# Performance work log

Measured on AMD Instinct MI355X. Metric: run time of the kernel, lower is better.

Reference implementation:

```python
import jax, jax.numpy as jnp
import numpy as np

B, T, F, H, E = 32, 512, 64, 64, 32  # batch, time, features(=sequence_length), hidden_dim, encoding_size


def setup_inputs() -> dict:
    key = jax.random.key(0)
    ks = jax.random.split(key, 14)
    sc = 0.05
    return {
        "x": jax.random.normal(ks[0], (B, T, F), jnp.float32),
        "s": jax.random.normal(ks[1], (B, T, E), jnp.float32),
        # gating FFN params
        "ffn_w1": jax.random.normal(ks[2], (F, H), jnp.float32) * sc,
        "ffn_b1": jnp.zeros((H,), jnp.float32),
        "ffn_w2": jax.random.normal(ks[3], (E, H), jnp.float32) * sc,
        "ffn_b2": jnp.zeros((H,), jnp.float32),
        "ffn_w3": jax.random.normal(ks[4], (H, F), jnp.float32) * sc,
        "ffn_b3": jnp.zeros((F,), jnp.float32),
        # per-feature expert FFN_j params (F experts, each Dense(1->H), ELU, Dense(H->H))
        "exp_w1": jax.random.normal(ks[5], (F, H), jnp.float32) * sc,  # weight of Dense(1->H) per feature
        "exp_b1": jnp.zeros((F, H), jnp.float32),
        "exp_w3": jax.random.normal(ks[6], (F, H, H), jnp.float32) * sc,
        "exp_b3": jnp.zeros((F, H), jnp.float32),
    }


def reference(x, s, ffn_w1, ffn_b1, ffn_w2, ffn_b2, ffn_w3, ffn_b3,
              exp_w1, exp_b1, exp_w3, exp_b3):
    # gating network: softmax over feature axis
    g = jnp.einsum('btf,fh->bth', x, ffn_w1) + ffn_b1 \
        + jnp.einsum('bte,eh->bth', s, ffn_w2) + ffn_b2
    logits = jnp.einsum('bth,hf->btf', jax.nn.elu(g), ffn_w3) + ffn_b3
    w_t = jax.nn.softmax(logits, axis=2)  # [B,T,F]

    # per-feature experts, batched: Dense(1->H) is a rank-1 outer product
    h = jax.nn.elu(x[..., None] * exp_w1[None, None] + exp_b1[None, None])  # [B,T,F,H]
    expert_out = jnp.einsum('btfh,fhk->btfk', h, exp_w3) + exp_b3[None, None]  # [B,T,F,H]

    # gate-weighted sum over features
    return jnp.einsum('btfk,btf->btk', expert_out, w_t)  # [B,T,H]
```

## Files before the change

### kernel.cpp

```cpp
#include <hip/hip_runtime.h>
#include <hip/hip_bf16.h>
#include <math.h>

#define NTOK 16384
#define LOG2E 1.44269504088896340736f
#define LN2   0.69314718055994530942f

typedef __attribute__((ext_vector_type(8))) short short8;
typedef __attribute__((ext_vector_type(4))) float f32x4;

__device__ __forceinline__ unsigned pack_bf16(float a, float b) {
    union { __hip_bfloat162 h; unsigned u; } cv;
    cv.h = __float22bfloat162_rn(make_float2(a, b));
    return cv.u;
}
__device__ __forceinline__ unsigned pk_bf16(float a, float b) {
    unsigned r;
    asm("v_cvt_pk_bf16_f32 %0, %1, %2" : "=v"(r) : "v"(a), "v"(b));
    return r;
}
__device__ __forceinline__ float exp2_hw(float x) {
#if __has_builtin(__builtin_amdgcn_exp2f)
    return __builtin_amdgcn_exp2f(x);
#else
    return __expf(x * LN2);
#endif
}
__device__ __forceinline__ float eluf(float z) {
    return z > 0.0f ? z : (__expf(z) - 1.0f);
}

__device__ __forceinline__ void agen16t(const float* __restrict__ wb,
                                        float xv, float wt, float wtln2,
                                        short8& A0, short8& A1) {
    auto site = [&](float w, float b) -> float {
        const float z2 = fmaf(xv, w, b);
        const float e  = exp2_hw(fminf(z2, 0.0f));
        return fmaf(wtln2, fmaxf(z2, 0.0f), fmaf(wt, e, -wt));
    };
    {
        const float4 wa  = *(const float4*)(wb);
        const float4 wv2 = *(const float4*)(wb + 4);
        const float4 ba  = *(const float4*)(wb + 64);
        const float4 bb  = *(const float4*)(wb + 68);
        uint4 v0;
        v0.x = pk_bf16(site(wa.x,  ba.x), site(wa.y,  ba.y));
        v0.y = pk_bf16(site(wa.z,  ba.z), site(wa.w,  ba.w));
        v0.z = pk_bf16(site(wv2.x, bb.x), site(wv2.y, bb.y));
        v0.w = pk_bf16(site(wv2.z, bb.z), site(wv2.w, bb.w));
        A0 = *(short8*)&v0;
    }
    {
        const float4 wc = *(const float4*)(wb + 32);
        const float4 wd = *(const float4*)(wb + 36);
        const float4 bc = *(const float4*)(wb + 96);
        const float4 bd = *(const float4*)(wb + 100);
        uint4 v1;
        v1.x = pk_bf16(site(wc.x, bc.x), site(wc.y, bc.y));
        v1.y = pk_bf16(site(wc.z, bc.z), site(wc.w, bc.w));
        v1.z = pk_bf16(site(wd.x, bd.x), site(wd.y, bd.y));
        v1.w = pk_bf16(site(wd.z, bd.z), site(wd.w, bd.w));
        A1 = *(short8*)&v1;
    }
}

__global__ __launch_bounds__(256)
void prepass(const float* __restrict__ ew3, const float* __restrict__ eb3,
             unsigned short* __restrict__ ws) {
    __shared__ float tile[64 * 65];
    const int bid = blockIdx.x, tid = threadIdx.x;
    const float* src = (bid < 64) ? (ew3 + (size_t)bid * 4096) : eb3;

    const int r = tid >> 2, c0 = (tid & 3) * 16;
    #pragma unroll
    for (int j = 0; j < 4; ++j) {
        float4 v = *(const float4*)(src + r * 64 + c0 + j * 4);
        tile[r * 65 + c0 + j * 4 + 0] = v.x;
        tile[r * 65 + c0 + j * 4 + 1] = v.y;
        tile[r * 65 + c0 + j * 4 + 2] = v.z;
        tile[r * 65 + c0 + j * 4 + 3] = v.w;
    }
    __syncthreads();

    uint4* dst = (uint4*)(ws + (size_t)bid * 4096);
    #pragma unroll
    for (int it = 0; it < 2; ++it) {
        const int idx = tid + it * 256;
        const int c = idx >> 8, u = (idx >> 6) & 3, l = idx & 63;
        const int mm = l & 15, q = (l >> 4) & 3;
        const int rb = c * 32 + q * 8, col = u * 16 + mm;
        unsigned pw[4];
        #pragma unroll
        for (int p = 0; p < 4; ++p)
            pw[p] = pack_bf16(tile[(rb + 2 * p) * 65 + col],
                              tile[(rb + 2 * p + 1) * 65 + col]);
        uint4 pk; pk.x = pw[0]; pk.y = pw[1]; pk.z = pw[2]; pk.w = pw[3];
        dst[idx] = pk;
    }
}

__global__ __launch_bounds__(256)
void prep_gate(const float* __restrict__ ew3, const float* __restrict__ eb3,
               const float* __restrict__ x,   const float* __restrict__ s,
               const float* __restrict__ fw1, const float* __restrict__ fb1,
               const float* __restrict__ fw2, const float* __restrict__ fb2,
               const float* __restrict__ fw3, const float* __restrict__ fb3,
               unsigned short* __restrict__ img, float* __restrict__ wtg)
{
    __shared__ float smem[64 * 65];
    const int tid = threadIdx.x;

    if (blockIdx.x < 65) {
        const int bid = blockIdx.x;
        const float* src = (bid < 64) ? (ew3 + (size_t)bid * 4096) : eb3;
        const int r = tid >> 2, c0 = (tid & 3) * 16;
        #pragma unroll
        for (int j = 0; j < 4; ++j) {
            float4 v = *(const float4*)(src + r * 64 + c0 + j * 4);
            smem[r * 65 + c0 + j * 4 + 0] = v.x;
            smem[r * 65 + c0 + j * 4 + 1] = v.y;
            smem[r * 65 + c0 + j * 4 + 2] = v.z;
            smem[r * 65 + c0 + j * 4 + 3] = v.w;
        }
        __syncthreads();
        uint4* dst = (uint4*)(img + (size_t)bid * 4096);
        #pragma unroll
        for (int it = 0; it < 2; ++it) {
            const int idx = tid + it * 256;
            const int c = idx >> 8, u = (idx >> 6) & 3, l = idx & 63;
            const int mm = l & 15, q = (l >> 4) & 3;
            const int rb = c * 32 + q * 8, col = u * 16 + mm;
            unsigned pw[4];
            #pragma unroll
            for (int p = 0; p < 4; ++p)
                pw[p] = pack_bf16(smem[(rb + 2 * p) * 65 + col],
                                  smem[(rb + 2 * p + 1) * 65 + col]);
            uint4 pk; pk.x = pw[0]; pk.y = pw[1]; pk.z = pw[2]; pk.w = pw[3];
            dst[idx] = pk;
        }
        return;
    }

    float* xls = smem;
    float* egs = smem + 16 * 68;
    const int gb = blockIdx.x - 65;
    const int tokbase = gb * 16;
    const int wv = tid >> 6, lane = tid & 63;

    {
        const int t = tid >> 4, fq = (tid & 15) * 4;
        *(float4*)&xls[t * 68 + fq] =
            *(const float4*)(x + (size_t)(tokbase + t) * 64 + fq);
    }
    __syncthreads();

    const int t0w = wv * 4;
    const float* sw = s + (size_t)(tokbase + t0w) * 32;
    float g[4];
    const float b0 = fb1[lane] + fb2[lane];
    #pragma unroll
    for (int t = 0; t < 4; ++t) g[t] = b0;
    #pragma unroll 2
    for (int f = 0; f < 64; f += 4) {
        const float w0 = fw1[(f + 0) * 64 + lane];
        const float w1 = fw1[(f + 1) * 64 + lane];
        const float w2 = fw1[(f + 2) * 64 + lane];
        const float w3v = fw1[(f + 3) * 64 + lane];
        #pragma unroll
        for (int t = 0; t < 4; ++t) {
            const float4 xa = *(const float4*)&xls[(t0w + t) * 68 + f];
            g[t] = fmaf(xa.x, w0, fmaf(xa.y, w1, fmaf(xa.z, w2, fmaf(xa.w, w3v, g[t]))));
        }
    }
    #pragma unroll 2
    for (int e = 0; e < 32; e += 4) {
        const float w0 = fw2[(e + 0) * 64 + lane];
        const float w1 = fw2[(e + 1) * 64 + lane];
        const float w2 = fw2[(e + 2) * 64 + lane];
        const float w3v = fw2[(e + 3) * 64 + lane];
        #pragma unroll
        for (int t = 0; t < 4; ++t) {
            const float4 sa = *(const float4*)(sw + t * 32 + e);
            g[t] = fmaf(sa.x, w0, fmaf(sa.y, w1, fmaf(sa.z, w2, fmaf(sa.w, w3v, g[t]))));
        }
    }
    #pragma unroll
    for (int t = 0; t < 4; ++t) egs[(t0w + t) * 64 + lane] = eluf(g[t]);

    float lg[4];
    const float b3 = fb3[lane];
    #pragma unroll
    for (int t = 0; t < 4; ++t) lg[t] = b3;
    #pragma unroll 2
    for (int h = 0; h < 64; h += 4) {
        const float w0 = fw3[(h + 0) * 64 + lane];
        const float w1 = fw3[(h + 1) * 64 + lane];
        const float w2 = fw3[(h + 2) * 64 + lane];
        const float w3v = fw3[(h + 3) * 64 + lane];
        #pragma unroll
        for (int t = 0; t < 4; ++t) {
            const float4 ev = *(const float4*)&egs[(t0w + t) * 64 + h];
            lg[t] = fmaf(ev.x, w0, fmaf(ev.y, w1, fmaf(ev.z, w2, fmaf(ev.w, w3v, lg[t]))));
        }
    }
    #pragma unroll
    for (int t = 0; t < 4; ++t) {
        float mx = lg[t];
        #pragma unroll
        for (int off = 32; off > 0; off >>= 1) mx = fmaxf(mx, __shfl_xor(mx, off));
        const float p = __expf(lg[t] - mx);
        float sm = p;
        #pragma unroll
        for (int off = 32; off > 0; off >>= 1) sm += __shfl_xor(sm, off);
        wtg[(size_t)(tokbase + t0w + t) * 64 + lane] = p / sm;
    }
}

__global__ __launch_bounds__(512, 4)
void moe_main8(const float* __restrict__ x,
               const float* __restrict__ ew1, const float* __restrict__ eb1,
               const unsigned short* __restrict__ img,
               const float* __restrict__ wtg,
               float* __restrict__ out)
{
    __shared__ __align__(16) float xls[32 * 68];
    __shared__ __align__(16) float wls[32 * 68];
    __shared__ __align__(16) float wbped[64 * 128];

    const int tid = threadIdx.x;
    const int wv = tid >> 6, lane = tid & 63;
    const int m = tid & 15, quad = (tid >> 4) & 3;
    const int tile = wv & 1, g = wv >> 1;
    const int f0 = g * 16;
    const int trow = tile * 16 + m;
    const int tokbase = blockIdx.x * 32;

    {
        const int t = tid >> 4, fq = (tid & 15) * 4;
        *(float4*)&xls[t * 68 + fq] =
            *(const float4*)(x + (size_t)(tokbase + t) * 64 + fq);
        *(float4*)&wls[t * 68 + fq] =
            *(const float4*)(wtg + (size_t)(tokbase + t) * 64 + fq);
        #pragma unroll
        for (int k = 0; k < 2; ++k) {
            const int idx = tid + k * 512;
            const int fr = idx >> 4, c4 = (idx & 15) * 4;
            float4 wv4 = *(const float4*)(ew1 + fr * 64 + c4);
            float4 bv4 = *(const float4*)(eb1 + fr * 64 + c4);
            wv4.x *= LOG2E; wv4.y *= LOG2E; wv4.z *= LOG2E; wv4.w *= LOG2E;
            bv4.x *= LOG2E; bv4.y *= LOG2E; bv4.z *= LOG2E; bv4.w *= LOG2E;
            *(float4*)&wbped[fr * 128 + c4]      = wv4;
            *(float4*)&wbped[fr * 128 + 64 + c4] = bv4;
        }
    }
    __syncthreads();

    f32x4 acc[4];
    #pragma unroll
    for (int u = 0; u < 4; ++u) acc[u] = (f32x4){0.f, 0.f, 0.f, 0.f};

    const uint4* bp = (const uint4*)img + (size_t)f0 * 512 + lane;
    uint4 B0[8], B1[8];
    #pragma unroll
    for (int j = 0; j < 8; ++j) B0[j] = bp[j * 64];
    bp += 512;

    const float* xp    = &xls[trow * 68 + f0];
    const float* wp    = &wls[trow * 68 + f0];
    const float* wbase = &wbped[f0 * 128 + quad * 8];
    float xvA = xp[0], wtA = wp[0], wlA = wtA * LN2;

    #pragma unroll 1
    for (int p = 0; p < 8; ++p) {
        #pragma unroll
        for (int j = 0; j < 8; ++j) B1[j] = bp[j * 64];
        bp += 512;
        const float xvB = xp[1], wtB = wp[1], wlB = wtB * LN2;
        {
            short8 a0, a1;
            agen16t(wbase, xvA, wtA, wlA, a0, a1);
            acc[0] = __builtin_amdgcn_mfma_f32_16x16x32_bf16(a0, *(short8*)&B0[0], acc[0], 0, 0, 0);
            acc[1] = __builtin_amdgcn_mfma_f32_16x16x32_bf16(a0, *(short8*)&B0[1], acc[1], 0, 0, 0);
            acc[2] = __builtin_amdgcn_mfma_f32_16x16x32_bf16(a0, *(short8*)&B0[2], acc[2], 0, 0, 0);
            acc[3] = __builtin_amdgcn_mfma_f32_16x16x32_bf16(a0, *(short8*)&B0[3], acc[3], 0, 0, 0);
            acc[0] = __builtin_amdgcn_mfma_f32_16x16x32_bf16(a1, *(short8*)&B0[4], acc[0], 0, 0, 0);
            acc[1] = __builtin_amdgcn_mfma_f32_16x16x32_bf16(a1, *(short8*)&B0[5], acc[1], 0, 0, 0);
            acc[2] = __builtin_amdgcn_mfma_f32_16x16x32_bf16(a1, *(short8*)&B0[6], acc[2], 0, 0, 0);
            acc[3] = __builtin_amdgcn_mfma_f32_16x16x32_bf16(a1, *(short8*)&B0[7], acc[3], 0, 0, 0);
        }
        wbase += 128;

        #pragma unroll
        for (int j = 0; j < 8; ++j) B0[j] = bp[j * 64];
        bp += 512;
        xvA = xp[2]; wtA = wp[2]; wlA = wtA * LN2;
        {
            short8 a0, a1;
            agen16t(wbase, xvB, wtB, wlB, a0, a1);
            acc[0] = __builtin_amdgcn_mfma_f32_16x16x32_bf16(a0, *(short8*)&B1[0], acc[0], 0, 0, 0);
            acc[1] = __builtin_amdgcn_mfma_f32_16x16x32_bf16(a0, *(short8*)&B1[1], acc[1], 0, 0, 0);
            acc[2] = __builtin_amdgcn_mfma_f32_16x16x32_bf16(a0, *(short8*)&B1[2], acc[2], 0, 0, 0);
            acc[3] = __builtin_amdgcn_mfma_f32_16x16x32_bf16(a0, *(short8*)&B1[3], acc[3], 0, 0, 0);
            acc[0] = __builtin_amdgcn_mfma_f32_16x16x32_bf16(a1, *(short8*)&B1[4], acc[0], 0, 0, 0);
            acc[1] = __builtin_amdgcn_mfma_f32_16x16x32_bf16(a1, *(short8*)&B1[5], acc[1], 0, 0, 0);
            acc[2] = __builtin_amdgcn_mfma_f32_16x16x32_bf16(a1, *(short8*)&B1[6], acc[2], 0, 0, 0);
            acc[3] = __builtin_amdgcn_mfma_f32_16x16x32_bf16(a1, *(short8*)&B1[7], acc[3], 0, 0, 0);
        }
        wbase += 128; xp += 2; wp += 2;
    }

    if (wv < 4) {
        const int eh = g;
        const int e0 = eh * 32 + quad * 8;
        uint4 av;
        av.x = pk_bf16(wls[trow * 68 + e0 + 0], wls[trow * 68 + e0 + 1]);
        av.y = pk_bf16(wls[trow * 68 + e0 + 2], wls[trow * 68 + e0 + 3]);
        av.z = pk_bf16(wls[trow * 68 + e0 + 4], wls[trow * 68 + e0 + 5]);
        av.w = pk_bf16(wls[trow * 68 + e0 + 6], wls[trow * 68 + e0 + 7]);
        const short8 a = *(short8*)&av;
        const uint4* bq = (const uint4*)img + (size_t)64 * 512 + lane;
        #pragma unroll
        for (int u = 0; u < 4; ++u) {
            uint4 bv = bq[eh * 256 + u * 64];
            acc[u] = __builtin_amdgcn_mfma_f32_16x16x32_bf16(a, *(short8*)&bv, acc[u], 0, 0, 0);
        }
    }

    __syncthreads();
    if (g >= 2) {
        float* p = wbped + tile * 2176 + (g - 2) * 1088;
        #pragma unroll
        for (int u = 0; u < 4; ++u)
            #pragma unroll
            for (int r = 0; r < 4; ++r)
                p[(quad * 4 + r) * 68 + u * 16 + m] = acc[u][r];
    }
    __syncthreads();
    if (g < 2) {
        const float* p = wbped + tile * 2176 + g * 1088;
        #pragma unroll
        for (int u = 0; u < 4; ++u)
            #pragma unroll
            for (int r = 0; r < 4; ++r)
                acc[u][r] += p[(quad * 4 + r) * 68 + u * 16 + m];
    }
    __syncthreads();
    if (g == 1) {
        float* p = wbped + tile * 2176;
        #pragma unroll
        for (int u = 0; u < 4; ++u)
            #pragma unroll
            for (int r = 0; r < 4; ++r)
                p[(quad * 4 + r) * 68 + u * 16 + m] = acc[u][r];
    }
    __syncthreads();
    if (g == 0) {
        float* p = wbped + tile * 2176;
        #pragma unroll
        for (int u = 0; u < 4; ++u)
            #pragma unroll
            for (int r = 0; r < 4; ++r) {
                const int idx = (quad * 4 + r) * 68 + u * 16 + m;
                p[idx] += acc[u][r];
            }
    }
    __syncthreads();

    {
        const int t = tid >> 4, kq = tid & 15;
        const float* srcp = wbped + (t >> 4) * 2176 + (t & 15) * 68 + kq * 4;
        *(float4*)(out + (size_t)(tokbase + t) * 64 + kq * 4) = *(const float4*)srcp;
    }
}

__global__ __launch_bounds__(512, 4)
void moe_main(const float* __restrict__ x,   const float* __restrict__ s,
              const float* __restrict__ fw1, const float* __restrict__ fb1,
              const float* __restrict__ fw2, const float* __restrict__ fb2,
              const float* __restrict__ fw3, const float* __restrict__ fb3,
              const float* __restrict__ ew1, const float* __restrict__ eb1,
              const float* __restrict__ ew3, const float* __restrict__ eb3,
              const unsigned short* __restrict__ img,
              float* __restrict__ out)
{
    __shared__ __align__(16) float xls[32 * 68];
    __shared__ __align__(16) float wts[32 * 65];
    __shared__ __align__(16) float egs[32 * 64];
    __shared__ __align__(16) float ped0[4][16 * 68];
    __shared__ __align__(16) float ped1[4][16 * 68];

    const int tid = threadIdx.x;
    const int wv = tid >> 6, lane = tid & 63;
    const int m = tid & 15, quad = (tid >> 4) & 3;
    const int tokbase = blockIdx.x * 32;

    {
        const int t = tid >> 4, fq = (tid & 15) * 4;
        *(float4*)&xls[t * 68 + fq] =
            *(const float4*)(x + (size_t)(tokbase + t) * 64 + fq);
    }
    __syncthreads();

    {
        const int t0w = wv * 4;
        const float* sw = s + (size_t)(tokbase + t0w) * 32;
        float g[4];
        const float b0 = fb1[lane] + fb2[lane];
        #pragma unroll
        for (int t = 0; t < 4; ++t) g[t] = b0;
        for (int f = 0; f < 64; f += 4) {
            const float w0 = fw1[(f + 0) * 64 + lane];
            const float w1 = fw1[(f + 1) * 64 + lane];
            const float w2 = fw1[(f + 2) * 64 + lane];
            const float w3v = fw1[(f + 3) * 64 + lane];
            #pragma unroll
            for (int t = 0; t < 4; ++t) {
                const float4 xa = *(const float4*)&xls[(t0w + t) * 68 + f];
                g[t] = fmaf(xa.x, w0, fmaf(xa.y, w1, fmaf(xa.z, w2, fmaf(xa.w, w3v, g[t]))));
            }
        }
        for (int e = 0; e < 32; e += 4) {
            const float w0 = fw2[(e + 0) * 64 + lane];
            const float w1 = fw2[(e + 1) * 64 + lane];
            const float w2 = fw2[(e + 2) * 64 + lane];
            const float w3v = fw2[(e + 3) * 64 + lane];
            #pragma unroll
            for (int t = 0; t < 4; ++t) {
                const float4 sa = *(const float4*)(sw + t * 32 + e);
                g[t] = fmaf(sa.x, w0, fmaf(sa.y, w1, fmaf(sa.z, w2, fmaf(sa.w, w3v, g[t]))));
            }
        }
        #pragma unroll
        for (int t = 0; t < 4; ++t) egs[(t0w + t) * 64 + lane] = eluf(g[t]);

        float lg[4];
        const float b3 = fb3[lane];
        #pragma unroll
        for (int t = 0; t < 4; ++t) lg[t] = b3;
        for (int h = 0; h < 64; h += 4) {
            const float w0 = fw3[(h + 0) * 64 + lane];
            const float w1 = fw3[(h + 1) * 64 + lane];
            const float w2 = fw3[(h + 2) * 64 + lane];
            const float w3v = fw3[(h + 3) * 64 + lane];
            #pragma unroll
            for (int t = 0; t < 4; ++t) {
                const float4 ev = *(const float4*)&egs[(t0w + t) * 64 + h];
                lg[t] = fmaf(ev.x, w0, fmaf(ev.y, w1, fmaf(ev.z, w2, fmaf(ev.w, w3v, lg[t]))));
            }
        }
        #pragma unroll
        for (int t = 0; t < 4; ++t) {
            float mx = lg[t];
            #pragma unroll
            for (int off = 32; off > 0; off >>= 1) mx = fmaxf(mx, __shfl_xor(mx, off));
            const float p = __expf(lg[t] - mx);
            float sm = p;
            #pragma unroll
            for (int off = 32; off > 0; off >>= 1) sm += __shfl_xor(sm, off);
            wts[(t0w + t) * 65 + lane] = p / sm;
        }
    }
    __syncthreads();

    const int f0 = wv * 8;
    f32x4 acc0[4], acc1[4];
    #pragma unroll
    for (int u = 0; u < 4; ++u) {
        acc0[u] = (f32x4){0.f, 0.f, 0.f, 0.f};
        acc1[u] = (f32x4){0.f, 0.f, 0.f, 0.f};
    }

    const uint4* bp = (const uint4*)img + (size_t)f0 * 512 + lane;
    uint4  B[2][8];
    float4 W[2][4];
    float4 Bb[2][4];
    float  XV[2][2];
    float  WT[2][2];

    #pragma unroll
    for (int i = 0; i < 8; ++i) B[0][i] = bp[(i >> 2) * 256 + (i & 3) * 64];
    bp += 512;
    #pragma unroll
    for (int c = 0; c < 2; ++c) {
        W[0][c * 2 + 0]  = *(const float4*)(ew1 + f0 * 64 + c * 32 + quad * 8);
        W[0][c * 2 + 1]  = *(const float4*)(ew1 + f0 * 64 + c * 32 + quad * 8 + 4);
        Bb[0][c * 2 + 0] = *(const float4*)(eb1 + f0 * 64 + c * 32 + quad * 8);
        Bb[0][c * 2 + 1] = *(const float4*)(eb1 + f0 * 64 + c * 32 + quad * 8 + 4);
    }
    XV[0][0] = xls[m * 68 + f0];        WT[0][0] = wts[m * 65 + f0];
    XV[0][1] = xls[(16 + m) * 68 + f0]; WT[0][1] = wts[(16 + m) * 65 + f0];

    #pragma unroll
    for (int ff = 0; ff < 8; ++ff) {
        const int cur = ff & 1, nxt = cur ^ 1;
        if (ff < 7) {
            const int fn = f0 + ff + 1;
            #pragma unroll
            for (int i = 0; i < 8; ++i) B[nxt][i] = bp[(i >> 2) * 256 + (i & 3) * 64];
            bp += 512;
            #pragma unroll
            for (int c = 0; c < 2; ++c) {
                W[nxt][c * 2 + 0]  = *(const float4*)(ew1 + fn * 64 + c * 32 + quad * 8);
                W[nxt][c * 2 + 1]  = *(const float4*)(ew1 + fn * 64 + c * 32 + quad * 8 + 4);
                Bb[nxt][c * 2 + 0] = *(const float4*)(eb1 + fn * 64 + c * 32 + quad * 8);
                Bb[nxt][c * 2 + 1] = *(const float4*)(eb1 + fn * 64 + c * 32 + quad * 8 + 4);
            }
            XV[nxt][0] = xls[m * 68 + fn];        WT[nxt][0] = wts[m * 65 + fn];
            XV[nxt][1] = xls[(16 + m) * 68 + fn]; WT[nxt][1] = wts[(16 + m) * 65 + fn];
        }
        const float xv0 = XV[cur][0], wt0 = WT[cur][0];
        const float xv1 = XV[cur][1], wt1 = WT[cur][1];
        short8 a0[2], a1[2];
        #pragma unroll
        for (int c = 0; c < 2; ++c) {
            const float4 wa = W[cur][c * 2 + 0],  wb = W[cur][c * 2 + 1];
            const float4 ba = Bb[cur][c * 2 + 0], bb = Bb[cur][c * 2 + 1];
            uint4 v0, v1;
            v0.x = pack_bf16(wt0 * eluf(fmaf(xv0, wa.x, ba.x)),
                             wt0 * eluf(fmaf(xv0, wa.y, ba.y)));
            v0.y = pack_bf16(wt0 * eluf(fmaf(xv0, wa.z, ba.z)),
                             wt0 * eluf(fmaf(xv0, wa.w, ba.w)));
            v0.z = pack_bf16(wt0 * eluf(fmaf(xv0, wb.x, bb.x)),
                             wt0 * eluf(fmaf(xv0, wb.y, bb.y)));
            v0.w = pack_bf16(wt0 * eluf(fmaf(xv0, wb.z, bb.z)),
                             wt0 * eluf(fmaf(xv0, wb.w, bb.w)));
            v1.x = pack_bf16(wt1 * eluf(fmaf(xv1, wa.x, ba.x)),
                             wt1 * eluf(fmaf(xv1, wa.y, ba.y)));
            v1.y = pack_bf16(wt1 * eluf(fmaf(xv1, wa.z, ba.z)),
                             wt1 * eluf(fmaf(xv1, wa.w, ba.w)));
            v1.z = pack_bf16(wt1 * eluf(fmaf(xv1, wb.x, bb.x)),
                             wt1 * eluf(fmaf(xv1, wb.y, bb.y)));
            v1.w = pack_bf16(wt1 * eluf(fmaf(xv1, wb.z, bb.z)),
                             wt1 * eluf(fmaf(xv1, wb.w, bb.w)));
            a0[c] = *(short8*)&v0;
            a1[c] = *(short8*)&v1;
        }
        acc0[0] = __builtin_amdgcn_mfma_f32_16x16x32_bf16(a0[0], *(short8*)&B[cur][0], acc0[0], 0, 0, 0);
        acc0[1] = __builtin_amdgcn_mfma_f32_16x16x32_bf16(a0[0], *(short8*)&B[cur][1], acc0[1], 0, 0, 0);
        acc0[2] = __builtin_amdgcn_mfma_f32_16x16x32_bf16(a0[0], *(short8*)&B[cur][2], acc0[2], 0, 0, 0);
        acc0[3] = __builtin_amdgcn_mfma_f32_16x16x32_bf16(a0[0], *(short8*)&B[cur][3], acc0[3], 0, 0, 0);
        acc1[0] = __builtin_amdgcn_mfma_f32_16x16x32_bf16(a1[0], *(short8*)&B[cur][0], acc1[0], 0, 0, 0);
        acc1[1] = __builtin_amdgcn_mfma_f32_16x16x32_bf16(a1[0], *(short8*)&B[cur][1], acc1[1], 0, 0, 0);
        acc1[2] = __builtin_amdgcn_mfma_f32_16x16x32_bf16(a1[0], *(short8*)&B[cur][2], acc1[2], 0, 0, 0);
        acc1[3] = __builtin_amdgcn_mfma_f32_16x16x32_bf16(a1[0], *(short8*)&B[cur][3], acc1[3], 0, 0, 0);
        acc0[0] = __builtin_amdgcn_mfma_f32_16x16x32_bf16(a0[1], *(short8*)&B[cur][4], acc0[0], 0, 0, 0);
        acc0[1] = __builtin_amdgcn_mfma_f32_16x16x32_bf16(a0[1], *(short8*)&B[cur][5], acc0[1], 0, 0, 0);
        acc0[2] = __builtin_amdgcn_mfma_f32_16x16x32_bf16(a0[1], *(short8*)&B[cur][6], acc0[2], 0, 0, 0);
        acc0[3] = __builtin_amdgcn_mfma_f32_16x16x32_bf16(a0[1], *(short8*)&B[cur][7], acc0[3], 0, 0, 0);
        acc1[0] = __builtin_amdgcn_mfma_f32_16x16x32_bf16(a1[1], *(short8*)&B[cur][4], acc1[0], 0, 0, 0);
        acc1[1] = __builtin_amdgcn_mfma_f32_16x16x32_bf16(a1[1], *(short8*)&B[cur][5], acc1[1], 0, 0, 0);
        acc1[2] = __builtin_amdgcn_mfma_f32_16x16x32_bf16(a1[1], *(short8*)&B[cur][6], acc1[2], 0, 0, 0);
        acc1[3] = __builtin_amdgcn_mfma_f32_16x16x32_bf16(a1[1], *(short8*)&B[cur][7], acc1[3], 0, 0, 0);
    }

    if (wv < 4) {
        const int tile = wv >> 1, eh = wv & 1;
        const int e0 = eh * 32 + quad * 8;
        const int trow = tile * 16 + m;
        uint4 av;
        av.x = pack_bf16(wts[trow * 65 + e0 + 0], wts[trow * 65 + e0 + 1]);
        av.y = pack_bf16(wts[trow * 65 + e0 + 2], wts[trow * 65 + e0 + 3]);
        av.z = pack_bf16(wts[trow * 65 + e0 + 4], wts[trow * 65 + e0 + 5]);
        av.w = pack_bf16(wts[trow * 65 + e0 + 6], wts[trow * 65 + e0 + 7]);
        short8 a = *(short8*)&av;
        const uint4* bq = (const uint4*)img + (size_t)64 * 512;
        if (tile == 0) {
            #pragma unroll
            for (int u = 0; u < 4; ++u) {
                uint4 bv = bq[eh * 256 + u * 64 + lane];
                acc0[u] = __builtin_amdgcn_mfma_f32_16x16x32_bf16(a, *(short8*)&bv, acc0[u], 0, 0, 0);
            }
        } else {
            #pragma unroll
            for (int u = 0; u < 4; ++u) {
                uint4 bv = bq[eh * 256 + u * 64 + lane];
                acc1[u] = __builtin_amdgcn_mfma_f32_16x16x32_bf16(a, *(short8*)&bv, acc1[u], 0, 0, 0);
            }
        }
    }

    if (wv >= 4) {
        #pragma unroll
        for (int u = 0; u < 4; ++u)
            #pragma unroll
            for (int r = 0; r < 4; ++r) {
                const int idx = (quad * 4 + r) * 68 + u * 16 + m;
                ped0[wv - 4][idx] = acc0[u][r];
                ped1[wv - 4][idx] = acc1[u][r];
            }
    }
    __syncthreads();
    if (wv < 4) {
        #pragma unroll
        for (int u = 0; u < 4; ++u)
            #pragma unroll
            for (int r = 0; r < 4; ++r) {
                const int idx = (quad * 4 + r) * 68 + u * 16 + m;
                acc0[u][r] += ped0[wv][idx];
                acc1[u][r] += ped1[wv][idx];
            }
    }
    __syncthreads();
    if (wv == 2 || wv == 3) {
        #pragma unroll
        for (int u = 0; u < 4; ++u)
            #pragma unroll
            for (int r = 0; r < 4; ++r) {
                const int idx = (quad * 4 + r) * 68 + u * 16 + m;
                ped0[wv - 2][idx] = acc0[u][r];
                ped1[wv - 2][idx] = acc1[u][r];
            }
    }
    __syncthreads();
    if (wv < 2) {
        #pragma unroll
        for (int u = 0; u < 4; ++u)
            #pragma unroll
            for (int r = 0; r < 4; ++r) {
                const int idx = (quad * 4 + r) * 68 + u * 16 + m;
                acc0[u][r] += ped0[wv][idx];
                acc1[u][r] += ped1[wv][idx];
            }
    }
    __syncthreads();
    if (wv == 1) {
        #pragma unroll
        for (int u = 0; u < 4; ++u)
            #pragma unroll
            for (int r = 0; r < 4; ++r) {
                const int idx = (quad * 4 + r) * 68 + u * 16 + m;
                ped0[0][idx] = acc0[u][r];
                ped1[0][idx] = acc1[u][r];
            }
    }
    __syncthreads();
    if (wv == 0) {
        #pragma unroll
        for (int u = 0; u < 4; ++u)
            #pragma unroll
            for (int r = 0; r < 4; ++r) {
                const int idx = (quad * 4 + r) * 68 + u * 16 + m;
                ped0[0][idx] += acc0[u][r];
                ped1[0][idx] += acc1[u][r];
            }
    }
    __syncthreads();

    {
        const int t = tid >> 4, kq = tid & 15;
        const float* srcp = (t < 16) ? &ped0[0][t * 68 + kq * 4]
                                     : &ped1[0][(t - 16) * 68 + kq * 4];
        *(float4*)(out + (size_t)(tokbase + t) * 64 + kq * 4) = *(const float4*)srcp;
    }
}

__device__ __forceinline__ void gen_a_fb(const float* __restrict__ ew1,
                                         const float* __restrict__ eb1,
                                         int f, int quad, float xv, float wt,
                                         short8* a) {
    #pragma unroll
    for (int c = 0; c < 2; ++c) {
        const float* w1p = ew1 + f * 64 + c * 32 + quad * 8;
        const float* b1p = eb1 + f * 64 + c * 32 + quad * 8;
        const float4 w1a = *(const float4*)w1p, w1b = *(const float4*)(w1p + 4);
        const float4 b1a = *(const float4*)b1p, b1b = *(const float4*)(b1p + 4);
        uint4 av;
        av.x = pack_bf16(wt * eluf(fmaf(xv, w1a.x, b1a.x)),
                         wt * eluf(fmaf(xv, w1a.y, b1a.y)));
        av.y = pack_bf16(wt * eluf(fmaf(xv, w1a.z, b1a.z)),
                         wt * eluf(fmaf(xv, w1a.w, b1a.w)));
        av.z = pack_bf16(wt * eluf(fmaf(xv, w1b.x, b1b.x)),
                         wt * eluf(fmaf(xv, w1b.y, b1b.y)));
        av.w = pack_bf16(wt * eluf(fmaf(xv, w1b.z, b1b.z)),
                         wt * eluf(fmaf(xv, w1b.w, b1b.w)));
        a[c] = *(short8*)&av;
    }
}
__device__ __forceinline__ void gen_b_fp32(const float* __restrict__ w3f,
                                           int quad, int m, short8 b[2][4]) {
    #pragma unroll
    for (int c = 0; c < 2; ++c)
        #pragma unroll
        for (int u = 0; u < 4; ++u) {
            const float* wp = w3f + (size_t)(c * 32 + quad * 8) * 64 + u * 16 + m;
            uint4 v;
            v.x = pack_bf16(wp[0],   wp[64]);
            v.y = pack_bf16(wp[128], wp[192]);
            v.z = pack_bf16(wp[256], wp[320]);
            v.w = pack_bf16(wp[384], wp[448]);
            b[c][u] = *(short8*)&v;
        }
}

__global__ __launch_bounds__(512, 8)
void moe_fb(const float* __restrict__ x,   const float* __restrict__ s,
            const float* __restrict__ fw1, const float* __restrict__ fb1,
            const float* __restrict__ fw2, const float* __restrict__ fb2,
            const float* __restrict__ fw3, const float* __restrict__ fb3,
            const float* __restrict__ ew1, const float* __restrict__ eb1,
            const float* __restrict__ ew3, const float* __restrict__ eb3,
            float* __restrict__ out)
{
    __shared__ __align__(16) float xls[16 * 68];
    __shared__ __align__(16) float wts[16 * 65];
    __shared__ __align__(16) float egs[16 * 64];
    __shared__ __align__(16) float ped[4][16 * 68];

    const int tid = threadIdx.x;
    const int wv = tid >> 6, lane = tid & 63;
    const int tokbase = blockIdx.x * 16;

    if (tid < 256) {
        const int t = tid >> 4, fq = (tid & 15) * 4;
        *(float4*)&xls[t * 68 + fq] =
            *(const float4*)(x + (size_t)(tokbase + t) * 64 + fq);
    }
    __syncthreads();
    {
        const int t0w = wv * 2;
        const float* sw = s + (size_t)(tokbase + t0w) * 32;
        float g0, g1;
        g0 = g1 = fb1[lane] + fb2[lane];
        for (int ff = 0; ff < 64; ff += 4) {
            const float4 xa = *(const float4*)&xls[(t0w + 0) * 68 + ff];
            const float4 xb = *(const float4*)&xls[(t0w + 1) * 68 + ff];
            const float w0 = fw1[(ff + 0) * 64 + lane];
            const float w1 = fw1[(ff + 1) * 64 + lane];
            const float w2 = fw1[(ff + 2) * 64 + lane];
            const float w3v = fw1[(ff + 3) * 64 + lane];
            g0 = fmaf(xa.x, w0, fmaf(xa.y, w1, fmaf(xa.z, w2, fmaf(xa.w, w3v, g0))));
            g1 = fmaf(xb.x, w0, fmaf(xb.y, w1, fmaf(xb.z, w2, fmaf(xb.w, w3v, g1))));
        }
        for (int e = 0; e < 32; e += 4) {
            const float4 sa = *(const float4*)(sw + e);
            const float4 sb = *(const float4*)(sw + 32 + e);
            const float w0 = fw2[(e + 0) * 64 + lane];
            const float w1 = fw2[(e + 1) * 64 + lane];
            const float w2 = fw2[(e + 2) * 64 + lane];
            const float w3v = fw2[(e + 3) * 64 + lane];
            g0 = fmaf(sa.x, w0, fmaf(sa.y, w1, fmaf(sa.z, w2, fmaf(sa.w, w3v, g0))));
            g1 = fmaf(sb.x, w0, fmaf(sb.y, w1, fmaf(sb.z, w2, fmaf(sb.w, w3v, g1))));
        }
        egs[(t0w + 0) * 64 + lane] = eluf(g0);
        egs[(t0w + 1) * 64 + lane] = eluf(g1);
        float lg0 = fb3[lane], lg1 = lg0;
        for (int h = 0; h < 64; h += 4) {
            const float4 e0 = *(const float4*)&egs[(t0w + 0) * 64 + h];
            const float4 e1 = *(const float4*)&egs[(t0w + 1) * 64 + h];
            const float w0 = fw3[(h + 0) * 64 + lane];
            const float w1 = fw3[(h + 1) * 64 + lane];
            const float w2 = fw3[(h + 2) * 64 + lane];
            const float w3v = fw3[(h + 3) * 64 + lane];
            lg0 = fmaf(e0.x, w0, fmaf(e0.y, w1, fmaf(e0.z, w2, fmaf(e0.w, w3v, lg0))));
            lg1 = fmaf(e1.x, w0, fmaf(e1.y, w1, fmaf(e1.z, w2, fmaf(e1.w, w3v, lg1))));
        }
        float mx0 = lg0, mx1 = lg1;
        #pragma unroll
        for (int off = 32; off > 0; off >>= 1) {
            mx0 = fmaxf(mx0, __shfl_xor(mx0, off));
            mx1 = fmaxf(mx1, __shfl_xor(mx1, off));
        }
        const float p0 = __expf(lg0 - mx0), p1 = __expf(lg1 - mx1);
        float s0 = p0, s1 = p1;
        #pragma unroll
        for (int off = 32; off > 0; off >>= 1) {
            s0 += __shfl_xor(s0, off);
            s1 += __shfl_xor(s1, off);
        }
        wts[(t0w + 0) * 65 + lane] = p0 / s0;
        wts[(t0w + 1) * 65 + lane] = p1 / s1;
    }
    __syncthreads();

    const int m = tid & 15, quad = (tid >> 4) & 3;
    const int f0 = wv * 8;
    f32x4 acc[4];
    #pragma unroll
    for (int u = 0; u < 4; ++u) acc[u] = (f32x4){0.f, 0.f, 0.f, 0.f};

    #pragma unroll
    for (int ff = 0; ff < 8; ++ff) {
        const int fcur = f0 + ff;
        short8 b[2][4], a[2];
        gen_b_fp32(ew3 + (size_t)fcur * 4096, quad, m, b);
        gen_a_fb(ew1, eb1, fcur, quad, xls[m * 68 + fcur], wts[m * 65 + fcur], a);
        #pragma unroll
        for (int u = 0; u < 4; ++u) {
            acc[u] = __builtin_amdgcn_mfma_f32_16x16x32_bf16(a[0], b[0][u], acc[u], 0, 0, 0);
            acc[u] = __builtin_amdgcn_mfma_f32_16x16x32_bf16(a[1], b[1][u], acc[u], 0, 0, 0);
        }
    }
    if (wv < 2) {
        const int e0 = wv * 32 + quad * 8;
        uint4 av;
        av.x = pack_bf16(wts[m * 65 + e0 + 0], wts[m * 65 + e0 + 1]);
        av.y = pack_bf16(wts[m * 65 + e0 + 2], wts[m * 65 + e0 + 3]);
        av.z = pack_bf16(wts[m * 65 + e0 + 4], wts[m * 65 + e0 + 5]);
        av.w = pack_bf16(wts[m * 65 + e0 + 6], wts[m * 65 + e0 + 7]);
        short8 a = *(short8*)&av;
        #pragma unroll
        for (int u = 0; u < 4; ++u) {
            const float* wp = eb3 + (size_t)e0 * 64 + u * 16 + m;
            uint4 bv;
            bv.x = pack_bf16(wp[0],   wp[64]);
            bv.y = pack_bf16(wp[128], wp[192]);
            bv.z = pack_bf16(wp[256], wp[320]);
            bv.w = pack_bf16(wp[384], wp[448]);
            acc[u] = __builtin_amdgcn_mfma_f32_16x16x32_bf16(a, *(short8*)&bv, acc[u], 0, 0, 0);
        }
    }
    if (wv >= 4) {
        #pragma unroll
        for (int u = 0; u < 4; ++u)
            #pragma unroll
            for (int r = 0; r < 4; ++r)
                ped[wv - 4][(quad * 4 + r) * 68 + u * 16 + m] = acc[u][r];
    }
    __syncthreads();
    if (wv < 4) {
        #pragma unroll
        for (int u = 0; u < 4; ++u)
            #pragma unroll
            for (int r = 0; r < 4; ++r)
                acc[u][r] += ped[wv][(quad * 4 + r) * 68 + u * 16 + m];
    }
    __syncthreads();
    if (wv == 2 || wv == 3) {
        #pragma unroll
        for (int u = 0; u < 4; ++u)
            #pragma unroll
            for (int r = 0; r < 4; ++r)
                ped[wv - 2][(quad * 4 + r) * 68 + u * 16 + m] = acc[u][r];
    }
    __syncthreads();
    if (wv < 2) {
        #pragma unroll
        for (int u = 0; u < 4; ++u)
            #pragma unroll
            for (int r = 0; r < 4; ++r)
                acc[u][r] += ped[wv][(quad * 4 + r) * 68 + u * 16 + m];
    }
    __syncthreads();
    if (wv == 1) {
        #pragma unroll
        for (int u = 0; u < 4; ++u)
            #pragma unroll
            for (int r = 0; r < 4; ++r)
                ped[0][(quad * 4 + r) * 68 + u * 16 + m] = acc[u][r];
    }
    __syncthreads();
    if (wv == 0) {
        #pragma unroll
        for (int u = 0; u < 4; ++u)
            #pragma unroll
            for (int r = 0; r < 4; ++r)
                ped[0][(quad * 4 + r) * 68 + u * 16 + m] += acc[u][r];
    }
    __syncthreads();
    if (tid < 256) {
        const int t = tid >> 4, kq = tid & 15;
        float4 o = *(const float4*)&ped[0][t * 68 + kq * 4];
        *(float4*)(out + (size_t)(tokbase + t) * 64 + kq * 4) = o;
    }
}

extern "C" void kernel_launch(void* const* d_in, const int* in_sizes, int n_in,
                              void* d_out, int out_size, void* d_ws, size_t ws_size,
                              hipStream_t stream) {
    const float* x   = (const float*)d_in[0];
    const float* s   = (const float*)d_in[1];
    const float* fw1 = (const float*)d_in[2];
    const float* fb1 = (const float*)d_in[3];
    const float* fw2 = (const float*)d_in[4];
    const float* fb2 = (const float*)d_in[5];
    const float* fw3 = (const float*)d_in[6];
    const float* fb3 = (const float*)d_in[7];
    const float* ew1 = (const float*)d_in[8];
    const float* eb1 = (const float*)d_in[9];
    const float* ew3 = (const float*)d_in[10];
    const float* eb3 = (const float*)d_in[11];
    float* out = (float*)d_out;

    const size_t img_bytes = (size_t)65 * 4096 * sizeof(unsigned short);
    const size_t wt_bytes  = (size_t)NTOK * 64 * sizeof(float);
    const bool al16 = (((uintptr_t)d_ws & 15) == 0);

    if (ws_size >= img_bytes + wt_bytes && al16) {
        unsigned short* img = (unsigned short*)d_ws;
        float* wtg = (float*)((char*)d_ws + img_bytes);
        prep_gate<<<dim3(65 + NTOK / 16), dim3(256), 0, stream>>>(
            ew3, eb3, x, s, fw1, fb1, fw2, fb2, fw3, fb3, img, wtg);
        moe_main8<<<dim3(NTOK / 32), dim3(512), 0, stream>>>(
            x, ew1, eb1, img, wtg, out);
    } else if (ws_size >= img_bytes && al16) {
        unsigned short* img = (unsigned short*)d_ws;
        prepass<<<dim3(65), dim3(256), 0, stream>>>(ew3, eb3, img);
        moe_main<<<dim3(NTOK / 32), dim3(512), 0, stream>>>(
            x, s, fw1, fb1, fw2, fb2, fw3, fb3, ew1, eb1, ew3, eb3, img, out);
    } else {
        moe_fb<<<dim3(NTOK / 16), dim3(512), 0, stream>>>(
            x, s, fw1, fb1, fw2, fb2, fw3, fb3, ew1, eb1, ew3, eb3, out);
    }
}
```

Before: 112.9 us.

## Give each wave both token tiles over 8 features to reuse B fragments

```diff
diff --git a/kernel.cpp b/kernel.cpp
--- a/kernel.cpp
+++ b/kernel.cpp
@@ -30,37 +30,53 @@
     return z > 0.0f ? z : (__expf(z) - 1.0f);
 }
 
-__device__ __forceinline__ void agen16t(const float* __restrict__ wb,
-                                        float xv, float wt, float wtln2,
-                                        short8& A0, short8& A1) {
-    auto site = [&](float w, float b) -> float {
-        const float z2 = fmaf(xv, w, b);
-        const float e  = exp2_hw(fminf(z2, 0.0f));
-        return fmaf(wtln2, fmaxf(z2, 0.0f), fmaf(wt, e, -wt));
+__device__ __forceinline__ void agen16x2(const float* __restrict__ wb,
+        float xv0, float wt0, float wl0,
+        float xv1, float wt1, float wl1,
+        short8& A00, short8& A01, short8& A10, short8& A11) {
+    auto s0 = [&](float w, float b) -> float {
+        const float z = fmaf(xv0, w, b);
+        const float e = exp2_hw(fminf(z, 0.0f));
+        return fmaf(wl0, fmaxf(z, 0.0f), fmaf(wt0, e, -wt0));
+    };
+    auto s1 = [&](float w, float b) -> float {
+        const float z = fmaf(xv1, w, b);
+        const float e = exp2_hw(fminf(z, 0.0f));
+        return fmaf(wl1, fmaxf(z, 0.0f), fmaf(wt1, e, -wt1));
     };
     {
         const float4 wa  = *(const float4*)(wb);
         const float4 wv2 = *(const float4*)(wb + 4);
         const float4 ba  = *(const float4*)(wb + 64);
         const float4 bb  = *(const float4*)(wb + 68);
-        uint4 v0;
-        v0.x = pk_bf16(site(wa.x,  ba.x), site(wa.y,  ba.y));
-        v0.y = pk_bf16(site(wa.z,  ba.z), site(wa.w,  ba.w));
-        v0.z = pk_bf16(site(wv2.x, bb.x), site(wv2.y, bb.y));
-        v0.w = pk_bf16(site(wv2.z, bb.z), site(wv2.w, bb.w));
-        A0 = *(short8*)&v0;
+        uint4 v0, v1;
+        v0.x = pk_bf16(s0(wa.x,  ba.x), s0(wa.y,  ba.y));
+        v0.y = pk_bf16(s0(wa.z,  ba.z), s0(wa.w,  ba.w));
+        v0.z = pk_bf16(s0(wv2.x, bb.x), s0(wv2.y, bb.y));
+        v0.w = pk_bf16(s0(wv2.z, bb.z), s0(wv2.w, bb.w));
+        v1.x = pk_bf16(s1(wa.x,  ba.x), s1(wa.y,  ba.y));
+        v1.y = pk_bf16(s1(wa.z,  ba.z), s1(wa.w,  ba.w));
+        v1.z = pk_bf16(s1(wv2.x, bb.x), s1(wv2.y, bb.y));
+        v1.w = pk_bf16(s1(wv2.z, bb.z), s1(wv2.w, bb.w));
+        A00 = *(short8*)&v0;
+        A10 = *(short8*)&v1;
     }
     {
         const float4 wc = *(const float4*)(wb + 32);
         const float4 wd = *(const float4*)(wb + 36);
         const float4 bc = *(const float4*)(wb + 96);
         const float4 bd = *(const float4*)(wb + 100);
-        uint4 v1;
-        v1.x = pk_bf16(site(wc.x, bc.x), site(wc.y, bc.y));
-        v1.y = pk_bf16(site(wc.z, bc.z), site(wc.w, bc.w));
-        v1.z = pk_bf16(site(wd.x, bd.x), site(wd.y, bd.y));
-        v1.w = pk_bf16(site(wd.z, bd.z), site(wd.w, bd.w));
-        A1 = *(short8*)&v1;
+        uint4 v0, v1;
+        v0.x = pk_bf16(s0(wc.x, bc.x), s0(wc.y, bc.y));
+        v0.y = pk_bf16(s0(wc.z, bc.z), s0(wc.w, bc.w));
+        v0.z = pk_bf16(s0(wd.x, bd.x), s0(wd.y, bd.y));
+        v0.w = pk_bf16(s0(wd.z, bd.z), s0(wd.w, bd.w));
+        v1.x = pk_bf16(s1(wc.x, bc.x), s1(wc.y, bc.y));
+        v1.y = pk_bf16(s1(wc.z, bc.z), s1(wc.w, bc.w));
+        v1.z = pk_bf16(s1(wd.x, bd.x), s1(wd.y, bd.y));
+        v1.w = pk_bf16(s1(wd.z, bd.z), s1(wd.w, bd.w));
+        A01 = *(short8*)&v0;
+        A11 = *(short8*)&v1;
     }
 }
 
@@ -217,7 +233,7 @@
 }
 
 __global__ __launch_bounds__(512, 4)
-void moe_main8(const float* __restrict__ x,
+void moe_main9(const float* __restrict__ x,
                const float* __restrict__ ew1, const float* __restrict__ eb1,
                const unsigned short* __restrict__ img,
                const float* __restrict__ wtg,
@@ -230,9 +246,7 @@
     const int tid = threadIdx.x;
     const int wv = tid >> 6, lane = tid & 63;
     const int m = tid & 15, quad = (tid >> 4) & 3;
-    const int tile = wv & 1, g = wv >> 1;
-    const int f0 = g * 16;
-    const int trow = tile * 16 + m;
+    const int f0 = wv * 8;
     const int tokbase = blockIdx.x * 32;
 
     {
@@ -255,63 +269,56 @@
     }
     __syncthreads();
 
-    f32x4 acc[4];
-    #pragma unroll
-    for (int u = 0; u < 4; ++u) acc[u] = (f32x4){0.f, 0.f, 0.f, 0.f};
+    f32x4 acc0[4], acc1[4];
+    #pragma unroll
+    for (int u = 0; u < 4; ++u) {
+        acc0[u] = (f32x4){0.f, 0.f, 0.f, 0.f};
+        acc1[u] = (f32x4){0.f, 0.f, 0.f, 0.f};
+    }
 
     const uint4* bp = (const uint4*)img + (size_t)f0 * 512 + lane;
-    uint4 B0[8], B1[8];
-    #pragma unroll
-    for (int j = 0; j < 8; ++j) B0[j] = bp[j * 64];
-    bp += 512;
-
-    const float* xp    = &xls[trow * 68 + f0];
-    const float* wp    = &wls[trow * 68 + f0];
     const float* wbase = &wbped[f0 * 128 + quad * 8];
-    float xvA = xp[0], wtA = wp[0], wlA = wtA * LN2;
+    const float* xp0 = &xls[m * 68 + f0];
+    const float* wp0 = &wls[m * 68 + f0];
+    const float* xp1 = &xls[(16 + m) * 68 + f0];
+    const float* wp1 = &wls[(16 + m) * 68 + f0];
 
     #pragma unroll 1
     for (int p = 0; p < 8; ++p) {
-        #pragma unroll
-        for (int j = 0; j < 8; ++j) B1[j] = bp[j * 64];
+        uint4 B[8];
+        #pragma unroll
+        for (int j = 0; j < 8; ++j) B[j] = bp[j * 64];
         bp += 512;
-        const float xvB = xp[1], wtB = wp[1], wlB = wtB * LN2;
-        {
-            short8 a0, a1;
-            agen16t(wbase, xvA, wtA, wlA, a0, a1);
-            acc[0] = __builtin_amdgcn_mfma_f32_16x16x32_bf16(a0, *(short8*)&B0[0], acc[0], 0, 0, 0);
-            acc[1] = __builtin_amdgcn_mfma_f32_16x16x32_bf16(a0, *(short8*)&B0[1], acc[1], 0, 0, 0);
-            acc[2] = __builtin_amdgcn_mfma_f32_16x16x32_bf16(a0, *(short8*)&B0[2], acc[2], 0, 0, 0);
-            acc[3] = __builtin_amdgcn_mfma_f32_16x16x32_bf16(a0, *(short8*)&B0[3], acc[3], 0, 0, 0);
-            acc[0] = __builtin_amdgcn_mfma_f32_16x16x32_bf16(a1, *(short8*)&B0[4], acc[0], 0, 0, 0);
-            acc[1] = __builtin_amdgcn_mfma_f32_16x16x32_bf16(a1, *(short8*)&B0[5], acc[1], 0, 0, 0);
-            acc[2] = __builtin_amdgcn_mfma_f32_16x16x32_bf16(a1, *(short8*)&B0[6], acc[2], 0, 0, 0);
-            acc[3] = __builtin_amdgcn_mfma_f32_16x16x32_bf16(a1, *(short8*)&B0[7], acc[3], 0, 0, 0);
-        }
+
+        const float xv0 = xp0[p], wt0 = wp0[p], wl0 = wt0 * LN2;
+        const float xv1 = xp1[p], wt1 = wp1[p], wl1 = wt1 * LN2;
+
+        short8 a00, a01, a10, a11;
+        agen16x2(wbase, xv0, wt0, wl0, xv1, wt1, wl1, a00, a01, a10, a11);
         wbase += 128;
 
-        #pragma unroll
-        for (int j = 0; j < 8; ++j) B0[j] = bp[j * 64];
-        bp += 512;
-        xvA = xp[2]; wtA = wp[2]; wlA = wtA * LN2;
-        {
-            short8 a0, a1;
-            agen16t(wbase, xvB, wtB, wlB, a0, a1);
-            acc[0] = __builtin_amdgcn_mfma_f32_16x16x32_bf16(a0, *(short8*)&B1[0], acc[0], 0, 0, 0);
-            acc[1] = __builtin_amdgcn_mfma_f32_16x16x32_bf16(a0, *(short8*)&B1[1], acc[1], 0, 0, 0);
-            acc[2] = __builtin_amdgcn_mfma_f32_16x16x32_bf16(a0, *(short8*)&B1[2], acc[2], 0, 0, 0);
-            acc[3] = __builtin_amdgcn_mfma_f32_16x16x32_bf16(a0, *(short8*)&B1[3], acc[3], 0, 0, 0);
-            acc[0] = __builtin_amdgcn_mfma_f32_16x16x32_bf16(a1, *(short8*)&B1[4], acc[0], 0, 0, 0);
-            acc[1] = __builtin_amdgcn_mfma_f32_16x16x32_bf16(a1, *(short8*)&B1[5], acc[1], 0, 0, 0);
-            acc[2] = __builtin_amdgcn_mfma_f32_16x16x32_bf16(a1, *(short8*)&B1[6], acc[2], 0, 0, 0);
-            acc[3] = __builtin_amdgcn_mfma_f32_16x16x32_bf16(a1, *(short8*)&B1[7], acc[3], 0, 0, 0);
-        }
-        wbase += 128; xp += 2; wp += 2;
+        acc0[0] = __builtin_amdgcn_mfma_f32_16x16x32_bf16(a00, *(short8*)&B[0], acc0[0], 0, 0, 0);
+        acc0[1] = __builtin_amdgcn_mfma_f32_16x16x32_bf16(a00, *(short8*)&B[1], acc0[1], 0, 0, 0);
+        acc0[2] = __builtin_amdgcn_mfma_f32_16x16x32_bf16(a00, *(short8*)&B[2], acc0[2], 0, 0, 0);
+        acc0[3] = __builtin_amdgcn_mfma_f32_16x16x32_bf16(a00, *(short8*)&B[3], acc0[3], 0, 0, 0);
+        acc1[0] = __builtin_amdgcn_mfma_f32_16x16x32_bf16(a10, *(short8*)&B[0], acc1[0], 0, 0, 0);
+        acc1[1] = __builtin_amdgcn_mfma_f32_16x16x32_bf16(a10, *(short8*)&B[1], acc1[1], 0, 0, 0);
+        acc1[2] = __builtin_amdgcn_mfma_f32_16x16x32_bf16(a10, *(short8*)&B[2], acc1[2], 0, 0, 0);
+        acc1[3] = __builtin_amdgcn_mfma_f32_16x16x32_bf16(a10, *(short8*)&B[3], acc1[3], 0, 0, 0);
+        acc0[0] = __builtin_amdgcn_mfma_f32_16x16x32_bf16(a01, *(short8*)&B[4], acc0[0], 0, 0, 0);
+        acc0[1] = __builtin_amdgcn_mfma_f32_16x16x32_bf16(a01, *(short8*)&B[5], acc0[1], 0, 0, 0);
+        acc0[2] = __builtin_amdgcn_mfma_f32_16x16x32_bf16(a01, *(short8*)&B[6], acc0[2], 0, 0, 0);
+        acc0[3] = __builtin_amdgcn_mfma_f32_16x16x32_bf16(a01, *(short8*)&B[7], acc0[3], 0, 0, 0);
+        acc1[0] = __builtin_amdgcn_mfma_f32_16x16x32_bf16(a11, *(short8*)&B[4], acc1[0], 0, 0, 0);
+        acc1[1] = __builtin_amdgcn_mfma_f32_16x16x32_bf16(a11, *(short8*)&B[5], acc1[1], 0, 0, 0);
+        acc1[2] = __builtin_amdgcn_mfma_f32_16x16x32_bf16(a11, *(short8*)&B[6], acc1[2], 0, 0, 0);
+        acc1[3] = __builtin_amdgcn_mfma_f32_16x16x32_bf16(a11, *(short8*)&B[7], acc1[3], 0, 0, 0);
     }
 
     if (wv < 4) {
-        const int eh = g;
+        const int tile = wv >> 1, eh = wv & 1;
         const int e0 = eh * 32 + quad * 8;
+        const int trow = tile * 16 + m;
         uint4 av;
         av.x = pk_bf16(wls[trow * 68 + e0 + 0], wls[trow * 68 + e0 + 1]);
         av.y = pk_bf16(wls[trow * 68 + e0 + 2], wls[trow * 68 + e0 + 3]);
@@ -319,56 +326,108 @@
         av.w = pk_bf16(wls[trow * 68 + e0 + 6], wls[trow * 68 + e0 + 7]);
         const short8 a = *(short8*)&av;
         const uint4* bq = (const uint4*)img + (size_t)64 * 512 + lane;
-        #pragma unroll
-        for (int u = 0; u < 4; ++u) {
-            uint4 bv = bq[eh * 256 + u * 64];
-            acc[u] = __builtin_amdgcn_mfma_f32_16x16x32_bf16(a, *(short8*)&bv, acc[u], 0, 0, 0);
-        }
-    }
-
-    __syncthreads();
-    if (g >= 2) {
-        float* p = wbped + tile * 2176 + (g - 2) * 1088;
-        #pragma unroll
-        for (int u = 0; u < 4; ++u)
-            #pragma unroll
-            for (int r = 0; r < 4; ++r)
-                p[(quad * 4 + r) * 68 + u * 16 + m] = acc[u][r];
-    }
-    __syncthreads();
-    if (g < 2) {
-        const float* p = wbped + tile * 2176 + g * 1088;
-        #pragma unroll
-        for (int u = 0; u < 4; ++u)
-            #pragma unroll
-            for (int r = 0; r < 4; ++r)
-                acc[u][r] += p[(quad * 4 + r) * 68 + u * 16 + m];
-    }
-    __syncthreads();
-    if (g == 1) {
-        float* p = wbped + tile * 2176;
-        #pragma unroll
-        for (int u = 0; u < 4; ++u)
-            #pragma unroll
-            for (int r = 0; r < 4; ++r)
-                p[(quad * 4 + r) * 68 + u * 16 + m] = acc[u][r];
-    }
-    __syncthreads();
-    if (g == 0) {
-        float* p = wbped + tile * 2176;
-        #pragma unroll
-        for (int u = 0; u < 4; ++u)
-            #pragma unroll
-            for (int r = 0; r < 4; ++r) {
-                const int idx = (quad * 4 + r) * 68 + u * 16 + m;
-                p[idx] += acc[u][r];
+        if (tile == 0) {
+            #pragma unroll
+            for (int u = 0; u < 4; ++u) {
+                uint4 bv = bq[eh * 256 + u * 64];
+                acc0[u] = __builtin_amdgcn_mfma_f32_16x16x32_bf16(a, *(short8*)&bv, acc0[u], 0, 0, 0);
+            }
+        } else {
+            #pragma unroll
+            for (int u = 0; u < 4; ++u) {
+                uint4 bv = bq[eh * 256 + u * 64];
+                acc1[u] = __builtin_amdgcn_mfma_f32_16x16x32_bf16(a, *(short8*)&bv, acc1[u], 0, 0, 0);
+            }
+        }
+    }
+
+    __syncthreads();
+    if (wv >= 4) {
+        const int s = wv - 4;
+        float* p0 = wbped + s * 1088;
+        float* p1 = (s < 3) ? (wbped + 4352 + s * 1088) : xls;
+        #pragma unroll
+        for (int u = 0; u < 4; ++u)
+            #pragma unroll
+            for (int r = 0; r < 4; ++r) {
+                const int idx = (quad * 4 + r) * 68 + u * 16 + m;
+                p0[idx] = acc0[u][r];
+                p1[idx] = acc1[u][r];
+            }
+    }
+    __syncthreads();
+    if (wv < 4) {
+        const int s = wv;
+        const float* p0 = wbped + s * 1088;
+        const float* p1 = (s < 3) ? (wbped + 4352 + s * 1088) : xls;
+        #pragma unroll
+        for (int u = 0; u < 4; ++u)
+            #pragma unroll
+            for (int r = 0; r < 4; ++r) {
+                const int idx = (quad * 4 + r) * 68 + u * 16 + m;
+                acc0[u][r] += p0[idx];
+                acc1[u][r] += p1[idx];
+            }
+    }
+    __syncthreads();
+    if (wv == 2 || wv == 3) {
+        const int s = wv - 2;
+        float* p0 = wbped + s * 1088;
+        float* p1 = wbped + 4352 + s * 1088;
+        #pragma unroll
+        for (int u = 0; u < 4; ++u)
+            #pragma unroll
+            for (int r = 0; r < 4; ++r) {
+                const int idx = (quad * 4 + r) * 68 + u * 16 + m;
+                p0[idx] = acc0[u][r];
+                p1[idx] = acc1[u][r];
+            }
+    }
+    __syncthreads();
+    if (wv < 2) {
+        const float* p0 = wbped + wv * 1088;
+        const float* p1 = wbped + 4352 + wv * 1088;
+        #pragma unroll
+        for (int u = 0; u < 4; ++u)
+            #pragma unroll
+            for (int r = 0; r < 4; ++r) {
+                const int idx = (quad * 4 + r) * 68 + u * 16 + m;
+                acc0[u][r] += p0[idx];
+                acc1[u][r] += p1[idx];
+            }
+    }
+    __syncthreads();
+    if (wv == 1) {
+        float* p0 = wbped;
+        float* p1 = wbped + 4352;
+        #pragma unroll
+        for (int u = 0; u < 4; ++u)
+            #pragma unroll
+            for (int r = 0; r < 4; ++r) {
+                const int idx = (quad * 4 + r) * 68 + u * 16 + m;
+                p0[idx] = acc0[u][r];
+                p1[idx] = acc1[u][r];
+            }
+    }
+    __syncthreads();
+    if (wv == 0) {
+        float* p0 = wbped;
+        float* p1 = wbped + 4352;
+        #pragma unroll
+        for (int u = 0; u < 4; ++u)
+            #pragma unroll
+            for (int r = 0; r < 4; ++r) {
+                const int idx = (quad * 4 + r) * 68 + u * 16 + m;
+                p0[idx] += acc0[u][r];
+                p1[idx] += acc1[u][r];
             }
     }
     __syncthreads();
 
     {
         const int t = tid >> 4, kq = tid & 15;
-        const float* srcp = wbped + (t >> 4) * 2176 + (t & 15) * 68 + kq * 4;
+        const float* srcp = (t < 16) ? (wbped + t * 68 + kq * 4)
+                                     : (wbped + 4352 + (t - 16) * 68 + kq * 4);
         *(float4*)(out + (size_t)(tokbase + t) * 64 + kq * 4) = *(const float4*)srcp;
     }
 }
@@ -890,7 +949,7 @@
         float* wtg = (float*)((char*)d_ws + img_bytes);
         prep_gate<<<dim3(65 + NTOK / 16), dim3(256), 0, stream>>>(
             ew3, eb3, x, s, fw1, fb1, fw2, fb2, fw3, fb3, img, wtg);
-        moe_main8<<<dim3(NTOK / 32), dim3(512), 0, stream>>>(
+        moe_main9<<<dim3(NTOK / 32), dim3(512), 0, stream>>>(
             x, ew1, eb1, img, wtg, out);
     } else if (ws_size >= img_bytes && al16) {
         unsigned short* img = (unsigned short*)d_ws;
```

Result: no change. 113.2 us, median of 2 (+0.3%).
